# Performance work log

Hardware: AMD Instinct MI355X
Metric: run time of the kernel (lower is better)

## Reference

```python
import jax, jax.numpy as jnp
import numpy as np

B, S, N = 64, 32, 128            # batch, seq_len, padded nodes per graph
DV, DW, DH = 512, 300, 1024      # dim_v, dim_word, dim_hidden
CLS, T_CTRL, L = 1024, 12, 4     # cls_fc_dim, controller steps, stack_len
NQ, NA, NE, NATTR, M = 100, 28, 16, 1000, 6  # vocabs, edge cats, attrs, num modules
# module order: 0 NoOp, 1 Find(push), 2 Transform, 3 Filter, 4 And, 5 Describe

def _valid_mat():
    m = np.zeros((L, M), dtype=np.float32)
    for s in range(L):
        m[s, 0] = 1.0
        m[s, 1] = 1.0 if s < L - 1 else 0.0
        m[s, 2] = 1.0 if s >= 1 else 0.0
        m[s, 3] = 1.0 if s >= 1 else 0.0
        m[s, 4] = 1.0 if s >= 2 else 0.0
        m[s, 5] = 1.0 if s >= 1 else 0.0
    return jnp.asarray(m)

VALID_MAT = _valid_mat()

def setup_inputs() -> dict:
    key = jax.random.key(0)
    ks = jax.random.split(key, 24)
    nrm = lambda k, sh, sc: jax.random.normal(k, sh, jnp.float32) * sc
    inp = {}
    inp['questions'] = jax.random.randint(ks[0], (B, S), 0, NQ)
    inp['questions_len'] = jax.random.randint(ks[1], (B,), 8, S + 1)
    inp['conn'] = (jax.random.uniform(ks[2], (B, N, N)) < 0.2).astype(jnp.float32)
    inp['cat_mat'] = jax.random.randint(ks[3], (B, N, N), 0, NE)
    inp['v_idx'] = jax.random.randint(ks[4], (B, N), 0, NATTR)
    inp['attr_emb'] = nrm(ks[5], (NATTR, DV), 1.0 / np.sqrt(DV))
    inp['edge_cat_vectors'] = nrm(ks[6], (NE, DV), 1.0 / np.sqrt(DV))
    inp['enc_emb'] = nrm(ks[7], (NQ, DW), 1.0 / np.sqrt(DW))
    inp['Wx'] = nrm(ks[8], (DW, 4 * DH), 1.0 / np.sqrt(DW))
    inp['Wh'] = nrm(ks[9], (DH, 4 * DH), 1.0 / np.sqrt(DH))
    inp['b_lstm'] = jnp.zeros((4 * DH,), jnp.float32)
    inp['W_cq'] = nrm(ks[10], (2 * DH, DH), 1.0 / np.sqrt(2 * DH))
    inp['b_cq'] = jnp.zeros((DH,), jnp.float32)
    inp['W_mod'] = nrm(ks[11], (DH, M), 1.0 / np.sqrt(DH))
    inp['W_att'] = nrm(ks[12], (DH, DH), 1.0 / np.sqrt(DH))
    inp['W_q'] = nrm(ks[13], (DH, DV), np.sqrt(2.0 / DH))
    inp['b_q'] = jnp.zeros((DV,), jnp.float32)
    inp['W_find'] = nrm(ks[14], (DV, DV), 1.0 / np.sqrt(DV))
    inp['W_desc'] = nrm(ks[15], (DV, DV), 1.0 / np.sqrt(DV))
    inp['W_cls1'] = nrm(ks[16], (DV + DH, CLS), np.sqrt(2.0 / (DV + DH)))
    inp['b_cls1'] = jnp.zeros((CLS,), jnp.float32)
    inp['W_cls2'] = nrm(ks[17], (CLS, NA), np.sqrt(2.0 / CLS))
    inp['b_cls2'] = jnp.zeros((NA,), jnp.float32)
    return inp

def _read(st, p):
    return jnp.einsum('bnl,bl->bn', st, p)

def _write(st, p, a):
    pe = p[:, None, :]
    return a[:, :, None] * pe + st * (1.0 - pe)

def _ptr_fw(p):
    q = jnp.concatenate([jnp.zeros_like(p[:, :1]), p[:, :-1]], axis=1)
    return q.at[:, -1].add(p[:, -1])

def _ptr_bw(p):
    q = jnp.concatenate([p[:, 1:], jnp.zeros_like(p[:, :1])], axis=1)
    return q.at[:, 0].add(p[:, 0])

def reference(questions, questions_len, conn, cat_mat, v_idx, attr_emb,
              edge_cat_vectors, enc_emb, Wx, Wh, b_lstm, W_cq, b_cq, W_mod,
              W_att, W_q, b_q, W_find, W_desc, W_cls1, b_cls1, W_cls2, b_cls2):
    # ---- question encoder: embedding + LSTM over time-major sequence ----
    emb = enc_emb[questions].transpose(1, 0, 2)  # [S,B,DW]

    def lstm_step(carry, x):
        h, c = carry
        g = x @ Wx + h @ Wh + b_lstm
        i, f, gg, o = jnp.split(g, 4, axis=-1)
        c = jax.nn.sigmoid(f) * c + jax.nn.sigmoid(i) * jnp.tanh(gg)
        h = jax.nn.sigmoid(o) * jnp.tanh(c)
        return (h, c), h

    init = (jnp.zeros((B, DH), jnp.float32), jnp.zeros((B, DH), jnp.float32))
    _, outs = jax.lax.scan(lstm_step, init, emb)            # [S,B,DH]
    outs_b = outs.transpose(1, 0, 2)                         # [B,S,DH]
    q_hidden = outs_b[jnp.arange(B), questions_len - 1]      # last valid state

    mask = jnp.arange(S)[:, None] < questions_len[None, :]   # [S,B]
    feat = attr_emb[v_idx]                                   # [B,N,DV]
    bidx = jnp.arange(B)[:, None, None]

    att_stack = jnp.zeros((B, N, L), jnp.float32)
    stack_ptr = jnp.zeros((B, L), jnp.float32).at[:, 0].set(1.0)
    mem = jnp.zeros((B, DV), jnp.float32)
    c_ctrl = jnp.zeros((B, DH), jnp.float32)
    inv_sqrt_dv = 1.0 / np.sqrt(DV)

    for t in range(T_CTRL):
        # ---- controller step: module distribution + textual attention ----
        cq = jnp.tanh(jnp.concatenate([c_ctrl, q_hidden], axis=1) @ W_cq + b_cq)
        module_prob = jax.nn.softmax(cq @ W_mod, axis=-1)     # [B,M]
        al = jnp.einsum('sbh,bh->sb', outs, cq @ W_att)
        cv = jax.nn.softmax(jnp.where(mask, al, -1e9), axis=0)
        c_ctrl = jnp.einsum('sb,sbh->bh', cv, outs)
        c_i = jax.nn.relu(c_ctrl @ W_q + b_q)                 # [B,DV]

        # ---- validity masking of module distribution ----
        validity = jnp.round(stack_ptr @ VALID_MAT)           # [B,M]
        mp = module_prob * validity
        s = jnp.sum(mp, axis=1, keepdims=True)
        mp = mp / jnp.where(s > 0, s, 1.0)

        # ---- run every module, soft-average by module prob ----
        a_find = jax.nn.sigmoid(jnp.einsum('bnd,bd->bn', feat @ W_find, c_i) * inv_sqrt_dv)
        a_in = _read(att_stack, stack_ptr)
        # Transform: edge-category-weighted message passing on graph
        we = jax.nn.softmax(c_i @ edge_cat_vectors.T, axis=-1)   # [B,NE]
        ew = we[bidx, cat_mat] * conn                            # [B,N,N]
        a_trans = jnp.minimum(jnp.einsum('bij,bj->bi', ew, a_in), 1.0)
        p_fw = _ptr_fw(stack_ptr)
        p_bw = _ptr_bw(stack_ptr)
        a_prev = _read(att_stack, p_bw)
        pooled = jnp.einsum('bn,bnd->bd', a_in, feat) / (jnp.sum(a_in, 1, keepdims=True) + 1e-6)
        res = [
            (att_stack, stack_ptr, mem),                                  # NoOp
            (_write(att_stack, p_fw, a_find), p_fw, mem),                 # Find (push)
            (_write(att_stack, stack_ptr, a_trans), stack_ptr, mem),      # Transform
            (_write(att_stack, stack_ptr, a_in * a_find), stack_ptr, mem),# Filter
            (_write(att_stack, p_bw, jnp.minimum(a_prev, a_in)), p_bw, mem),  # And (pop)
            (att_stack, p_bw, pooled @ W_desc),                           # Describe
        ]
        att_stack = jnp.einsum('bm,mbnl->bnl', mp, jnp.stack([r[0] for r in res]))
        stack_ptr = jnp.einsum('bm,mbl->bl', mp, jnp.stack([r[1] for r in res]))
        mem = jnp.einsum('bm,mbd->bd', mp, jnp.stack([r[2] for r in res]))

    final = jnp.concatenate([mem, q_hidden], axis=1)
    h1 = jax.nn.relu(final @ W_cls1 + b_cls1)
    logits = h1 @ W_cls2 + b_cls2
    return logits
```

## Files before the change

### kernel.cpp

```cpp
#include <hip/hip_runtime.h>
#include <math.h>

#define B 64
#define S 32
#define NN 128
#define DV 512
#define DW 300
#define DH 1024
#define CLS 1024
#define T_CTRL 12
#define LL 4
#define NA 28
#define NE 16
#define MM 6

__device__ __forceinline__ float sigmoidf_(float x) { return 1.0f / (1.0f + expf(-x)); }

template<bool TRANS, class AF, class WF>
__device__ __forceinline__ void gemm_core(int kbeg, int Kc, AF loadA, WF loadW,
                                          float* part, int Cld, int orow) {
  __shared__ float Ast[2][64 * 36];
  __shared__ float Ws[2][32 * 64];
  const int tid = threadIdx.x;
  const int j0 = blockIdx.x * 64;
  const int ntiles = Kc >> 5;
  const int rg = tid & 15, cg = tid >> 4;
  float4 av[2], wv[2];

  auto fetch = [&](int kt) {
    #pragma unroll
    for (int i2 = 0; i2 < 2; ++i2) {
      int idx = tid + i2 * 256;
      av[i2] = loadA(idx >> 3, kt + (idx & 7) * 4);
    }
    #pragma unroll
    for (int i2 = 0; i2 < 2; ++i2) {
      int idx = tid + i2 * 256;
      if (!TRANS) wv[i2] = loadW(kt + (idx >> 4), j0 + (idx & 15) * 4);
      else        wv[i2] = loadW(j0 + (idx >> 3), kt + (idx & 7) * 4);
    }
  };
  auto commit = [&](int buf) {
    #pragma unroll
    for (int i2 = 0; i2 < 2; ++i2) {
      int idx = tid + i2 * 256;
      *(float4*)&Ast[buf][(idx >> 3) * 36 + (idx & 7) * 4] = av[i2];
    }
    #pragma unroll
    for (int i2 = 0; i2 < 2; ++i2) {
      int idx = tid + i2 * 256;
      if (!TRANS) {
        *(float4*)&Ws[buf][(idx >> 4) * 64 + (idx & 15) * 4] = wv[i2];
      } else {
        int jloc = idx >> 3, k4 = (idx & 7) * 4;
        Ws[buf][(k4 + 0) * 64 + jloc] = wv[i2].x;
        Ws[buf][(k4 + 1) * 64 + jloc] = wv[i2].y;
        Ws[buf][(k4 + 2) * 64 + jloc] = wv[i2].z;
        Ws[buf][(k4 + 3) * 64 + jloc] = wv[i2].w;
      }
    }
  };

  float acc[4][4] = {};
  fetch(kbeg);
  commit(0);
  __syncthreads();
  for (int i = 0; i < ntiles; ++i) {
    if (i + 1 < ntiles) fetch(kbeg + (i + 1) * 32);
    const float* As = &Ast[i & 1][0];
    const float* Wp = &Ws[i & 1][0];
    #pragma unroll
    for (int kq = 0; kq < 8; ++kq) {
      float4 a0 = *(const float4*)&As[(rg     ) * 36 + kq * 4];
      float4 a1 = *(const float4*)&As[(rg + 16) * 36 + kq * 4];
      float4 a2 = *(const float4*)&As[(rg + 32) * 36 + kq * 4];
      float4 a3 = *(const float4*)&As[(rg + 48) * 36 + kq * 4];
      float4 w0 = *(const float4*)&Wp[(kq * 4 + 0) * 64 + cg * 4];
      float4 w1 = *(const float4*)&Wp[(kq * 4 + 1) * 64 + cg * 4];
      float4 w2 = *(const float4*)&Wp[(kq * 4 + 2) * 64 + cg * 4];
      float4 w3 = *(const float4*)&Wp[(kq * 4 + 3) * 64 + cg * 4];
      #define STEP(m, AV) \
        acc[m][0]=fmaf(AV.x,w0.x,acc[m][0]); acc[m][1]=fmaf(AV.x,w0.y,acc[m][1]); \
        acc[m][2]=fmaf(AV.x,w0.z,acc[m][2]); acc[m][3]=fmaf(AV.x,w0.w,acc[m][3]); \
        acc[m][0]=fmaf(AV.y,w1.x,acc[m][0]); acc[m][1]=fmaf(AV.y,w1.y,acc[m][1]); \
        acc[m][2]=fmaf(AV.y,w1.z,acc[m][2]); acc[m][3]=fmaf(AV.y,w1.w,acc[m][3]); \
        acc[m][0]=fmaf(AV.z,w2.x,acc[m][0]); acc[m][1]=fmaf(AV.z,w2.y,acc[m][1]); \
        acc[m][2]=fmaf(AV.z,w2.z,acc[m][2]); acc[m][3]=fmaf(AV.z,w2.w,acc[m][3]); \
        acc[m][0]=fmaf(AV.w,w3.x,acc[m][0]); acc[m][1]=fmaf(AV.w,w3.y,acc[m][1]); \
        acc[m][2]=fmaf(AV.w,w3.z,acc[m][2]); acc[m][3]=fmaf(AV.w,w3.w,acc[m][3]);
      STEP(0, a0) STEP(1, a1) STEP(2, a2) STEP(3, a3)
      #undef STEP
    }
    if (i + 1 < ntiles) { __syncthreads(); commit((i + 1) & 1); __syncthreads(); }
  }
  float* op = part + (size_t)orow * 64 * Cld + j0 + cg * 4;
  #pragma unroll
  for (int m = 0; m < 4; ++m)
    *(float4*)&op[(size_t)(rg + 16 * m) * Cld] = make_float4(acc[m][0], acc[m][1], acc[m][2], acc[m][3]);
}

__global__ void init_kernel(float* c_lstm, float* c_ctrl, float* att_stack, float* mem, float* sptr) {
  int idx = blockIdx.x * 256 + threadIdx.x;
  if (idx < B * DH) { c_lstm[idx] = 0.f; c_ctrl[idx] = 0.f; }
  if (idx < B * NN * LL) att_stack[idx] = 0.f;
  if (idx < B * DV) mem[idx] = 0.f;
  if (idx < B * LL) sptr[idx] = ((idx & (LL - 1)) == 0) ? 1.f : 0.f;
}

__global__ void embq_kernel(const int* __restrict__ questions, const float* __restrict__ enc_emb,
                            float* __restrict__ embq) {
  int row = blockIdx.x;
  int t = row >> 6, b = row & 63;
  int qid = questions[b * S + t];
  int c = threadIdx.x;
  embq[(size_t)row * 320 + c] = (c < DW) ? enc_emb[(size_t)qid * DW + c] : 0.f;
}

__global__ __launch_bounds__(256) void xpre_kernel(const float* __restrict__ embq,
                                                   const float* __restrict__ Wx,
                                                   float* __restrict__ Xbuf) {
  int t = blockIdx.y, ch = blockIdx.z;
  auto Al = [&](int r, int k) -> float4 {
    return *(const float4*)&embq[(size_t)(t * 64 + r) * 320 + k];
  };
  auto Wl = [&](int k, int j) -> float4 {
    if (k < 300) return *(const float4*)&Wx[(size_t)k * 4096 + j];
    return make_float4(0.f, 0.f, 0.f, 0.f);
  };
  gemm_core<false>(ch * 160, 160, Al, Wl, Xbuf + (size_t)t * 524288 + (size_t)ch * 262144, 4096, 0);
}

__global__ __launch_bounds__(256) void f2_kernel(const float* __restrict__ attr_emb,
                                                 const float* __restrict__ W_find,
                                                 float* __restrict__ F2) {
  auto Al = [&](int r, int k) -> float4 {
    int gr = blockIdx.y * 64 + r;
    if (gr > 999) gr = 999;
    return *(const float4*)&attr_emb[(size_t)gr * 512 + k];
  };
  auto Wl = [&](int k, int j) -> float4 { return *(const float4*)&W_find[(size_t)k * 512 + j]; };
  gemm_core<false>(0, 512, Al, Wl, F2, 512, blockIdx.y);
}

__global__ __launch_bounds__(256) void lstm_gemm_kernel(const float* __restrict__ h_prev,
                                                        const float* __restrict__ Wh,
                                                        float* __restrict__ part,
                                                        const float* __restrict__ embq,
                                                        const float* __restrict__ Wx,
                                                        float* __restrict__ Xbuf, int t) {
  if (blockIdx.y < 8) {
    auto Al = [&](int r, int k) -> float4 { return *(const float4*)&h_prev[(size_t)r * 1024 + k]; };
    auto Wl = [&](int k, int j) -> float4 { return *(const float4*)&Wh[(size_t)k * 4096 + j]; };
    gemm_core<false>(blockIdx.y * 128, 128, Al, Wl, part, 4096, blockIdx.y);
  } else {
    if (t == 31) return;
    int ch = blockIdx.y - 8;
    auto Al = [&](int r, int k) -> float4 {
      return *(const float4*)&embq[(size_t)((t + 1) * 64 + r) * 320 + k];
    };
    auto Wl = [&](int k, int j) -> float4 {
      if (k < 300) return *(const float4*)&Wx[(size_t)k * 4096 + j];
      return make_float4(0.f, 0.f, 0.f, 0.f);
    };
    gemm_core<false>(ch * 160, 160, Al, Wl,
                     Xbuf + (size_t)((t + 1) & 1) * 524288 + (size_t)ch * 262144, 4096, 0);
  }
}

__global__ __launch_bounds__(256) void lstm_gate_kernel(const float* __restrict__ part, int SK,
                                                        const float* __restrict__ px,
                                                        const float* __restrict__ b_lstm,
                                                        float* __restrict__ h_out, float* __restrict__ c_st) {
  int idx = blockIdx.x * 256 + threadIdx.x;
  int b = idx >> 10, j = idx & 1023;
  const float* x0 = px + (size_t)b * 4096;
  const float* x1 = px + 262144 + (size_t)b * 4096;
  float gi = x0[j] + x1[j];
  float gf = x0[1024 + j] + x1[1024 + j];
  float gg = x0[2048 + j] + x1[2048 + j];
  float go = x0[3072 + j] + x1[3072 + j];
  const float* pb = part + (size_t)b * 4096;
  for (int c = 0; c < SK; ++c) {
    const float* p = pb + (size_t)c * 262144;
    gi += p[j]; gf += p[1024 + j]; gg += p[2048 + j]; go += p[3072 + j];
  }
  gi += b_lstm[j]; gf += b_lstm[1024 + j]; gg += b_lstm[2048 + j]; go += b_lstm[3072 + j];
  float c = sigmoidf_(gf) * c_st[idx] + sigmoidf_(gi) * tanhf(gg);
  h_out[idx] = sigmoidf_(go) * tanhf(c);
  c_st[idx] = c;
}

__global__ __launch_bounds__(256) void c1_kernel(const float* __restrict__ c_ctrl,
                                                 const float* __restrict__ outs, const int* __restrict__ qlen,
                                                 const float* __restrict__ W_cq, float* __restrict__ partA,
                                                 const float* __restrict__ partE, const float* __restrict__ mp,
                                                 float* __restrict__ mem, int do_epi) {
  if (blockIdx.x == 16) {
    if (!do_epi) return;
    int t0 = blockIdx.y * 256 + threadIdx.x;
    #pragma unroll
    for (int i = 0; i < 4; ++i) {
      int f4 = t0 + i * 2048;
      int b = f4 >> 7, j = (f4 & 127) * 4;
      const float* m = &mp[b * 6];
      float s04 = m[0] + m[1] + m[2] + m[3] + m[4];
      float4 s = make_float4(0.f, 0.f, 0.f, 0.f);
      for (int c = 0; c < 8; ++c) {
        float4 v = *(const float4*)&partE[(size_t)c * 32768 + b * 512 + j];
        s.x += v.x; s.y += v.y; s.z += v.z; s.w += v.w;
      }
      float4 o = *(const float4*)&mem[b * 512 + j];
      o.x = s04 * o.x + m[5] * s.x; o.y = s04 * o.y + m[5] * s.y;
      o.z = s04 * o.z + m[5] * s.z; o.w = s04 * o.w + m[5] * s.w;
      *(float4*)&mem[b * 512 + j] = o;
    }
    return;
  }
  auto Al = [&](int r, int k) -> float4 {
    if (k < 1024) return *(const float4*)&c_ctrl[r * 1024 + k];
    int tq = qlen[r] - 1;
    return *(const float4*)&outs[(size_t)tq * 65536 + r * 1024 + (k - 1024)];
  };
  auto Wl = [&](int k, int j) -> float4 { return *(const float4*)&W_cq[(size_t)k * 1024 + j]; };
  gemm_core<false>(blockIdx.y * 256, 256, Al, Wl, partA, 1024, blockIdx.y);
}

__global__ __launch_bounds__(256) void c2_kernel(const float* __restrict__ partA,
                                                 const float* __restrict__ b_cq,
                                                 const float* __restrict__ W_att,
                                                 const float* __restrict__ W_mod,
                                                 float* __restrict__ partB) {
  auto Al = [&](int r, int k) -> float4 {
    float4 s = *(const float4*)&b_cq[k];
    for (int c = 0; c < 8; ++c) {
      float4 v = *(const float4*)&partA[(size_t)c * 65536 + r * 1024 + k];
      s.x += v.x; s.y += v.y; s.z += v.z; s.w += v.w;
    }
    return make_float4(tanhf(s.x), tanhf(s.y), tanhf(s.z), tanhf(s.w));
  };
  auto Wl = [&](int k, int j) -> float4 {
    if (j < 1024) return *(const float4*)&W_att[(size_t)k * 1024 + j];
    float v[4];
    #pragma unroll
    for (int i = 0; i < 4; ++i) {
      int jj = j + i;
      v[i] = (jj < 1030) ? W_mod[(size_t)k * 6 + (jj - 1024)] : 0.f;
    }
    return make_float4(v[0], v[1], v[2], v[3]);
  };
  gemm_core<false>(blockIdx.y * 64, 64, Al, Wl, partB, 1088, blockIdx.y);
}

__global__ __launch_bounds__(256) void attn_kernel(const float* __restrict__ partB,
                                                   const float* __restrict__ outs,
                                                   const int* __restrict__ qlen,
                                                   float* __restrict__ c_ctrl) {
  int b = blockIdx.x >> 2, hq = blockIdx.x & 3;
  int tid = threadIdx.x;
  __shared__ float aw[DH];
  __shared__ float alv[S];
  __shared__ float cvs[S];
  {
    int c4 = tid * 4;
    float4 s = make_float4(0.f, 0.f, 0.f, 0.f);
    for (int c = 0; c < 16; ++c) {
      float4 v = *(const float4*)&partB[(size_t)c * 69632 + b * 1088 + c4];
      s.x += v.x; s.y += v.y; s.z += v.z; s.w += v.w;
    }
    *(float4*)&aw[c4] = s;
  }
  __syncthreads();
  {
    int wv = tid >> 6, lane = tid & 63;
    #pragma unroll
    for (int u = 0; u < 4; ++u) {
      int s2 = wv * 4 + u;
      const float4* orow = (const float4*)&outs[(size_t)s2 * 65536 + b * 1024];
      float pr = 0.f;
      #pragma unroll
      for (int q = 0; q < 4; ++q) {
        float4 f = orow[lane + 64 * q];
        float4 w = *(const float4*)&aw[(lane + 64 * q) * 4];
        pr += f.x * w.x + f.y * w.y + f.z * w.z + f.w * w.w;
      }
      #pragma unroll
      for (int off = 32; off > 0; off >>= 1) pr += __shfl_xor(pr, off);
      if (lane == 0) alv[s2] = pr;
    }
  }
  __syncthreads();
  if (tid < 64) {
    int len = qlen[b];
    float v = (tid < S && tid < len) ? alv[tid] : -1e9f;
    float mx = v;
    #pragma unroll
    for (int off = 32; off > 0; off >>= 1) mx = fmaxf(mx, __shfl_xor(mx, off));
    float e = (tid < S && tid < len) ? expf(v - mx) : 0.f;
    float sm = e;
    #pragma unroll
    for (int off = 32; off > 0; off >>= 1) sm += __shfl_xor(sm, off);
    if (tid < S) cvs[tid] = e / sm;
  }
  __syncthreads();
  {
    int h = hq * 256 + tid;
    float a = 0.f;
    #pragma unroll 8
    for (int s2 = 0; s2 < S; ++s2)
      a = fmaf(cvs[s2], outs[(size_t)s2 * 65536 + b * 1024 + h], a);
    c_ctrl[b * 1024 + h] = a;
  }
}

__global__ __launch_bounds__(256) void c4_kernel(const float* __restrict__ c_ctrl,
                                                 const float* __restrict__ W_q,
                                                 float* __restrict__ partC) {
  auto Al = [&](int r, int k) -> float4 { return *(const float4*)&c_ctrl[r * 1024 + k]; };
  auto Wl = [&](int k, int j) -> float4 { return *(const float4*)&W_q[(size_t)k * 512 + j]; };
  gemm_core<false>(blockIdx.y * 64, 64, Al, Wl, partC, 512, blockIdx.y);
}

__global__ __launch_bounds__(256) void prep_kernel(const float* __restrict__ partC,
                                                   const float* __restrict__ partB,
                                                   const float* __restrict__ b_q,
                                                   const float* __restrict__ edge_cat,
                                                   const float* __restrict__ sptr_in,
                                                   const float* __restrict__ att_stack,
                                                   float* __restrict__ c_i, float* __restrict__ we,
                                                   float* __restrict__ mp, float* __restrict__ spv,
                                                   float* __restrict__ ain, float* __restrict__ aw4,
                                                   float* __restrict__ asum) {
  int b = blockIdx.x, tid = threadIdx.x;
  __shared__ float ci[512];
  __shared__ float lds[64];
  for (int col = tid; col < 512; col += 256) {
    float s = b_q[col];
    for (int c = 0; c < 16; ++c) s += partC[(size_t)c * 32768 + b * 512 + col];
    s = fmaxf(s, 0.f);
    ci[col] = s;
    c_i[b * 512 + col] = s;
  }
  if (tid < MM) {
    float s = 0.f;
    for (int c = 0; c < 16; ++c) s += partB[(size_t)c * 69632 + b * 1088 + 1024 + tid];
    lds[16 + tid] = s;
  }
  __syncthreads();
  {
    int wv = tid >> 6, lane = tid & 63;
    for (int e = wv; e < NE; e += 4) {
      const float* er = &edge_cat[(size_t)e * 512];
      float p = 0.f;
      #pragma unroll
      for (int q = 0; q < 8; ++q) p = fmaf(ci[lane + 64 * q], er[lane + 64 * q], p);
      #pragma unroll
      for (int off = 32; off > 0; off >>= 1) p += __shfl_xor(p, off);
      if (lane == 0) lds[e] = p;
    }
  }
  __syncthreads();
  if (tid == 0) {
    float mx = lds[0];
    for (int e = 1; e < NE; ++e) mx = fmaxf(mx, lds[e]);
    float sm = 0.f, ex[NE];
    for (int e = 0; e < NE; ++e) { ex[e] = expf(lds[e] - mx); sm += ex[e]; }
    for (int e = 0; e < NE; ++e) we[b * NE + e] = ex[e] / sm;
    float mx2 = lds[16];
    for (int m = 1; m < MM; ++m) mx2 = fmaxf(mx2, lds[16 + m]);
    float e6[MM], sm2 = 0.f;
    for (int m = 0; m < MM; ++m) { e6[m] = expf(lds[16 + m] - mx2); sm2 += e6[m]; }
    float p0 = sptr_in[b * 4 + 0], p1 = sptr_in[b * 4 + 1];
    float p2 = sptr_in[b * 4 + 2], p3 = sptr_in[b * 4 + 3];
    float sp[12];
    sp[0] = p0; sp[1] = p1; sp[2] = p2; sp[3] = p3;
    sp[4] = 0.f;      sp[5] = p0; sp[6] = p1; sp[7] = p2 + p3;
    sp[8] = p0 + p1;  sp[9] = p2; sp[10] = p3; sp[11] = 0.f;
    for (int i = 0; i < 12; ++i) { spv[b * 12 + i] = sp[i]; lds[22 + i] = sp[i]; }
    float val[MM];
    val[0] = rintf(p0 + p1 + p2 + p3);
    val[1] = rintf(p0 + p1 + p2);
    val[2] = rintf(p1 + p2 + p3);
    val[3] = val[2];
    val[4] = rintf(p2 + p3);
    val[5] = val[2];
    float mpv[MM], ssum = 0.f;
    #pragma unroll
    for (int m = 0; m < MM; ++m) { mpv[m] = (e6[m] / sm2) * val[m]; ssum += mpv[m]; }
    float inv = (ssum > 0.f) ? 1.f / ssum : 1.f;
    #pragma unroll
    for (int m = 0; m < MM; ++m) mp[b * MM + m] = mpv[m] * inv;
  }
  __syncthreads();
  if (tid < 128) {
    float4 st = *(const float4*)&att_stack[(b * NN + tid) * LL];
    float ainv = st.x * lds[22] + st.y * lds[23] + st.z * lds[24] + st.w * lds[25];
    float ap   = st.x * lds[30] + st.y * lds[31] + st.z * lds[32] + st.w * lds[33];
    ain[b * NN + tid] = ainv;
    aw4[b * NN + tid] = fminf(ap, ainv);
    float t2 = ainv;
    #pragma unroll
    for (int off = 32; off > 0; off >>= 1) t2 += __shfl_xor(t2, off);
    if ((tid & 63) == 0) lds[40 + (tid >> 6)] = t2;
  }
  __syncthreads();
  if (tid == 0) asum[b] = lds[40] + lds[41] + 1e-6f;
}

__global__ __launch_bounds__(256) void stackf_kernel(const int* __restrict__ v_idx,
                                                     const float* __restrict__ attr_emb,
                                                     const float* __restrict__ F2,
                                                     const float* __restrict__ c_i,
                                                     const float* __restrict__ we,
                                                     const int* __restrict__ cat_mat,
                                                     const float* __restrict__ conn,
                                                     const float* __restrict__ ain,
                                                     const float* __restrict__ asum,
                                                     float* __restrict__ afind,
                                                     float* __restrict__ atr,
                                                     float* __restrict__ pooled) {
  int job = blockIdx.x, tid = threadIdx.x;
  __shared__ float lds[192];
  if (job < 2048) {
    int gw = job * 4 + (tid >> 6);
    int b = gw >> 7, n = gw & 127, lane = tid & 63;
    int vid = v_idx[b * NN + n];
    const float4* fp = (const float4*)&F2[(size_t)vid * DV];
    const float4* up = (const float4*)&c_i[(size_t)b * DV];
    float pr = 0.f;
    #pragma unroll
    for (int q = 0; q < 2; ++q) {
      float4 f = fp[lane + 64 * q], u = up[lane + 64 * q];
      pr += f.x * u.x + f.y * u.y + f.z * u.z + f.w * u.w;
    }
    #pragma unroll
    for (int off = 32; off > 0; off >>= 1) pr += __shfl_xor(pr, off);
    if (lane == 0) afind[b * NN + n] = sigmoidf_(pr * 0.04419417382415922f);
  } else if (job < 2560) {
    int j2 = job - 2048;
    int b = j2 >> 3, ig = j2 & 7;
    if (tid < 128) lds[tid] = ain[b * NN + tid];
    else if (tid < 144) lds[tid] = we[b * NE + tid - 128];
    __syncthreads();
    int i = ig * 16 + (tid >> 4);
    const int* crow = &cat_mat[((size_t)b * NN + i) * NN];
    const float* nrow = &conn[((size_t)b * NN + i) * NN];
    float a = 0.f;
    #pragma unroll
    for (int q = 0; q < 8; ++q) {
      int j = (tid & 15) + 16 * q;
      a = fmaf(lds[128 + crow[j]] * nrow[j], lds[j], a);
    }
    a += __shfl_xor(a, 1); a += __shfl_xor(a, 2); a += __shfl_xor(a, 4); a += __shfl_xor(a, 8);
    if ((tid & 15) == 0) atr[b * NN + i] = fminf(a, 1.f);
  } else {
    int j3 = job - 2560;
    int b = j3 >> 1, d = (j3 & 1) * 256 + tid;
    int* vidL = (int*)&lds[128];
    if (tid < 128) { lds[tid] = ain[b * NN + tid]; vidL[tid] = v_idx[b * NN + tid]; }
    __syncthreads();
    float a = 0.f;
    #pragma unroll 4
    for (int n = 0; n < NN; ++n)
      a = fmaf(lds[n], attr_emb[(size_t)vidL[n] * DV + d], a);
    pooled[b * DV + d] = a / asum[b];
  }
}

__global__ __launch_bounds__(256) void c7u_kernel(const float* __restrict__ pooled,
                                                  const float* __restrict__ W_desc,
                                                  float* __restrict__ partE,
                                                  const float* __restrict__ spv,
                                                  const float* __restrict__ mp,
                                                  const float* __restrict__ afind,
                                                  const float* __restrict__ ain,
                                                  const float* __restrict__ atr,
                                                  const float* __restrict__ aw4,
                                                  float* __restrict__ att_stack,
                                                  float* __restrict__ sptr) {
  int tid = threadIdx.x;
  if (blockIdx.y < 8) {
    auto Al = [&](int r, int k) -> float4 { return *(const float4*)&pooled[r * 512 + k]; };
    auto Wl = [&](int k, int j) -> float4 { return *(const float4*)&W_desc[(size_t)k * 512 + j]; };
    gemm_core<false>(blockIdx.y * 64, 64, Al, Wl, partE, 512, blockIdx.y);
    return;
  }
  int b = (blockIdx.y - 8) * 8 + blockIdx.x;
  __shared__ float sp[12], smp[MM];
  if (tid < 12) sp[tid] = spv[b * 12 + tid];
  else if (tid < 12 + MM) smp[tid - 12] = mp[b * MM + (tid - 12)];
  __syncthreads();
  #pragma unroll
  for (int i = 0; i < 2; ++i) {
    int e = tid + i * 256;
    int n = e >> 2, l = e & 3;
    float st = att_stack[(b * NN + n) * LL + l];
    float keep = smp[0] + smp[5] + smp[1] * (1.f - sp[4 + l]) + (smp[2] + smp[3]) * (1.f - sp[l])
               + smp[4] * (1.f - sp[8 + l]);
    float add = sp[4 + l] * smp[1] * afind[b * NN + n]
              + sp[l] * (smp[2] * atr[b * NN + n] + smp[3] * ain[b * NN + n] * afind[b * NN + n])
              + sp[8 + l] * smp[4] * aw4[b * NN + n];
    att_stack[(b * NN + n) * LL + l] = keep * st + add;
  }
  if (tid < LL)
    sptr[b * LL + tid] = (smp[0] + smp[2] + smp[3]) * sp[tid] + smp[1] * sp[4 + tid]
                       + (smp[4] + smp[5]) * sp[8 + tid];
}

__global__ __launch_bounds__(256) void cl1_kernel(const float* __restrict__ partE,
                                                  const float* __restrict__ mp,
                                                  const float* __restrict__ mem,
                                                  const float* __restrict__ outs,
                                                  const int* __restrict__ qlen,
                                                  const float* __restrict__ W_cls1,
                                                  float* __restrict__ partH) {
  auto Al = [&](int r, int k) -> float4 {
    if (k < 512) {
      float4 s = make_float4(0.f, 0.f, 0.f, 0.f);
      for (int c = 0; c < 8; ++c) {
        float4 v = *(const float4*)&partE[(size_t)c * 32768 + r * 512 + k];
        s.x += v.x; s.y += v.y; s.z += v.z; s.w += v.w;
      }
      const float* m = &mp[r * 6];
      float s04 = m[0] + m[1] + m[2] + m[3] + m[4];
      float4 o = *(const float4*)&mem[r * 512 + k];
      return make_float4(s04 * o.x + m[5] * s.x, s04 * o.y + m[5] * s.y,
                         s04 * o.z + m[5] * s.z, s04 * o.w + m[5] * s.w);
    }
    int tq = qlen[r] - 1;
    return *(const float4*)&outs[(size_t)tq * 65536 + r * 1024 + (k - 512)];
  };
  auto Wl = [&](int k, int j) -> float4 { return *(const float4*)&W_cls1[(size_t)k * 1024 + j]; };
  gemm_core<false>(blockIdx.y * 192, 192, Al, Wl, partH, 1024, blockIdx.y);
}

__global__ __launch_bounds__(256) void cl2_kernel(const float* __restrict__ partH,
                                                  const float* __restrict__ b_cls1,
                                                  const float* __restrict__ W_cls2,
                                                  float* __restrict__ partJ) {
  auto Al = [&](int r, int k) -> float4 {
    float4 s = *(const float4*)&b_cls1[k];
    for (int c = 0; c < 8; ++c) {
      float4 v = *(const float4*)&partH[(size_t)c * 65536 + r * 1024 + k];
      s.x += v.x; s.y += v.y; s.z += v.z; s.w += v.w;
    }
    return make_float4(fmaxf(s.x, 0.f), fmaxf(s.y, 0.f), fmaxf(s.z, 0.f), fmaxf(s.w, 0.f));
  };
  auto Wl = [&](int k, int j) -> float4 {
    float v[4];
    #pragma unroll
    for (int i = 0; i < 4; ++i) { int jj = j + i; v[i] = (jj < NA) ? W_cls2[(size_t)k * NA + jj] : 0.f; }
    return make_float4(v[0], v[1], v[2], v[3]);
  };
  gemm_core<false>(blockIdx.y * 128, 128, Al, Wl, partJ, 64, blockIdx.y);
}

__global__ void cl3_kernel(const float* __restrict__ partJ, const float* __restrict__ b_cls2,
                           float* __restrict__ logits) {
  int idx = blockIdx.x * 256 + threadIdx.x;
  if (idx >= B * NA) return;
  int r = idx / NA, j = idx - r * NA;
  float s = b_cls2[j];
  for (int c = 0; c < 8; ++c) s += partJ[(size_t)c * 4096 + r * 64 + j];
  logits[idx] = s;
}

extern "C" void kernel_launch(void* const* d_in, const int* in_sizes, int n_in,
                              void* d_out, int out_size, void* d_ws, size_t ws_size,
                              hipStream_t stream) {
  const int*   questions = (const int*)d_in[0];
  const int*   qlen      = (const int*)d_in[1];
  const float* conn      = (const float*)d_in[2];
  const int*   cat_mat   = (const int*)d_in[3];
  const int*   v_idx     = (const int*)d_in[4];
  const float* attr_emb  = (const float*)d_in[5];
  const float* edge_cat  = (const float*)d_in[6];
  const float* enc_emb   = (const float*)d_in[7];
  const float* Wx        = (const float*)d_in[8];
  const float* Wh        = (const float*)d_in[9];
  const float* b_lstm    = (const float*)d_in[10];
  const float* W_cq      = (const float*)d_in[11];
  const float* b_cq      = (const float*)d_in[12];
  const float* W_mod     = (const float*)d_in[13];
  const float* W_att     = (const float*)d_in[14];
  const float* W_q       = (const float*)d_in[15];
  const float* b_q       = (const float*)d_in[16];
  const float* W_find    = (const float*)d_in[17];
  const float* W_desc    = (const float*)d_in[18];
  const float* W_cls1    = (const float*)d_in[19];
  const float* b_cls1    = (const float*)d_in[20];
  const float* W_cls2    = (const float*)d_in[21];
  const float* b_cls2    = (const float*)d_in[22];
  float* logits = (float*)d_out;

  float* w = (float*)d_ws;
  size_t off = 0;
  float* outs      = w + off; off += (size_t)S * B * DH;
  float* embq      = w + off; off += (size_t)S * B * 320;
  float* Xbuf      = w + off; off += 2 * 2 * 262144;
  float* F2        = w + off; off += 1024 * 512;
  float* share     = w + off; off += 2457600;
  float* partE     = w + off; off += 262144;
  float* partH     = w + off; off += 524288;
  float* partJ     = w + off; off += 32768;
  float* c_ctrl    = w + off; off += B * DH;
  float* c_lstm    = w + off; off += B * DH;
  float* ci_buf    = w + off; off += B * DV;
  float* we_buf    = w + off; off += B * NE;
  float* mp_buf    = w + off; off += B * MM;
  float* spv_buf   = w + off; off += B * 12;
  float* ain_buf   = w + off; off += B * NN;
  float* aw4_buf   = w + off; off += B * NN;
  float* afind_buf = w + off; off += B * NN;
  float* atr_buf   = w + off; off += B * NN;
  float* asum_buf  = w + off; off += B;
  float* att_stack = w + off; off += B * NN * LL;
  float* sptr_buf  = w + off; off += B * LL;
  float* mem       = w + off; off += B * DV;
  float* pooled    = w + off; off += B * DV;

  float* partLSTM = share;
  float* partA = share;
  float* partB = share + 524288;
  float* partC = share + 1638400;

  init_kernel<<<256, 256, 0, stream>>>(c_lstm, c_ctrl, att_stack, mem, sptr_buf);
  embq_kernel<<<S * B, 320, 0, stream>>>(questions, enc_emb, embq);
  xpre_kernel<<<dim3(64, 2, 2), 256, 0, stream>>>(embq, Wx, Xbuf);
  f2_kernel<<<dim3(8, 16), 256, 0, stream>>>(attr_emb, W_find, F2);

  lstm_gate_kernel<<<(B * DH) / 256, 256, 0, stream>>>(partLSTM, 0, Xbuf, b_lstm, outs, c_lstm);
  for (int t = 1; t < S; ++t) {
    lstm_gemm_kernel<<<dim3(64, 10), 256, 0, stream>>>(outs + (size_t)(t - 1) * B * DH, Wh,
                                                       partLSTM, embq, Wx, Xbuf, t);
    lstm_gate_kernel<<<(B * DH) / 256, 256, 0, stream>>>(partLSTM, 8, Xbuf + (size_t)(t & 1) * 524288,
                                                         b_lstm, outs + (size_t)t * B * DH, c_lstm);
  }

  for (int it = 0; it < T_CTRL; ++it) {
    c1_kernel<<<dim3(17, 8), 256, 0, stream>>>(c_ctrl, outs, qlen, W_cq, partA,
                                               partE, mp_buf, mem, it > 0 ? 1 : 0);
    c2_kernel<<<dim3(17, 16), 256, 0, stream>>>(partA, b_cq, W_att, W_mod, partB);
    attn_kernel<<<256, 256, 0, stream>>>(partB, outs, qlen, c_ctrl);
    c4_kernel<<<dim3(8, 16), 256, 0, stream>>>(c_ctrl, W_q, partC);
    prep_kernel<<<64, 256, 0, stream>>>(partC, partB, b_q, edge_cat, sptr_buf, att_stack,
                                        ci_buf, we_buf, mp_buf, spv_buf, ain_buf, aw4_buf, asum_buf);
    stackf_kernel<<<2688, 256, 0, stream>>>(v_idx, attr_emb, F2, ci_buf, we_buf, cat_mat, conn,
                                            ain_buf, asum_buf, afind_buf, atr_buf, pooled);
    c7u_kernel<<<dim3(8, 16), 256, 0, stream>>>(pooled, W_desc, partE, spv_buf, mp_buf,
                                                afind_buf, ain_buf, atr_buf, aw4_buf,
                                                att_stack, sptr_buf);
  }

  cl1_kernel<<<dim3(16, 8), 256, 0, stream>>>(partE, mp_buf, mem, outs, qlen, W_cls1, partH);
  cl2_kernel<<<dim3(1, 8), 256, 0, stream>>>(partH, b_cls1, W_cls2, partJ);
  cl3_kernel<<<7, 256, 0, stream>>>(partJ, b_cls2, logits);
}
```

Before: 1.575 ms.

## Precompute all LSTM input projections upfront and fuse W_q GEMM into prep kernel

Replaces the per-step overlapped input-projection GEMM with a single up-front GEMM over all 32 timesteps, stored in a full-size X buffer, so each recurrent step launches only the Wh GEMM. It also removes the separate c4 split-K GEMM kernel and computes c_ctrl·W_q directly inside prep_kernel with a per-batch-row dot-product loop. This cuts one launch per controller iteration and the partial-sum traffic. The cost is a scalar 1024x512 matvec per block in prep, run on only 64 blocks, which may be slower than the tiled GEMM it replaces.

```diff
diff --git a/kernel.cpp b/kernel.cpp
--- a/kernel.cpp
+++ b/kernel.cpp
@@ -116,18 +116,17 @@
   embq[(size_t)row * 320 + c] = (c < DW) ? enc_emb[(size_t)qid * DW + c] : 0.f;
 }
 
-__global__ __launch_bounds__(256) void xpre_kernel(const float* __restrict__ embq,
-                                                   const float* __restrict__ Wx,
-                                                   float* __restrict__ Xbuf) {
-  int t = blockIdx.y, ch = blockIdx.z;
+__global__ __launch_bounds__(256) void xgemm_kernel(const float* __restrict__ embq,
+                                                    const float* __restrict__ Wx,
+                                                    float* __restrict__ X) {
   auto Al = [&](int r, int k) -> float4 {
-    return *(const float4*)&embq[(size_t)(t * 64 + r) * 320 + k];
+    return *(const float4*)&embq[(size_t)(blockIdx.y * 64 + r) * 320 + k];
   };
   auto Wl = [&](int k, int j) -> float4 {
     if (k < 300) return *(const float4*)&Wx[(size_t)k * 4096 + j];
     return make_float4(0.f, 0.f, 0.f, 0.f);
   };
-  gemm_core<false>(ch * 160, 160, Al, Wl, Xbuf + (size_t)t * 524288 + (size_t)ch * 262144, 4096, 0);
+  gemm_core<false>(0, 320, Al, Wl, X, 4096, blockIdx.y);
 }
 
 __global__ __launch_bounds__(256) void f2_kernel(const float* __restrict__ attr_emb,
@@ -144,41 +143,20 @@
 
 __global__ __launch_bounds__(256) void lstm_gemm_kernel(const float* __restrict__ h_prev,
                                                         const float* __restrict__ Wh,
-                                                        float* __restrict__ part,
-                                                        const float* __restrict__ embq,
-                                                        const float* __restrict__ Wx,
-                                                        float* __restrict__ Xbuf, int t) {
-  if (blockIdx.y < 8) {
-    auto Al = [&](int r, int k) -> float4 { return *(const float4*)&h_prev[(size_t)r * 1024 + k]; };
-    auto Wl = [&](int k, int j) -> float4 { return *(const float4*)&Wh[(size_t)k * 4096 + j]; };
-    gemm_core<false>(blockIdx.y * 128, 128, Al, Wl, part, 4096, blockIdx.y);
-  } else {
-    if (t == 31) return;
-    int ch = blockIdx.y - 8;
-    auto Al = [&](int r, int k) -> float4 {
-      return *(const float4*)&embq[(size_t)((t + 1) * 64 + r) * 320 + k];
-    };
-    auto Wl = [&](int k, int j) -> float4 {
-      if (k < 300) return *(const float4*)&Wx[(size_t)k * 4096 + j];
-      return make_float4(0.f, 0.f, 0.f, 0.f);
-    };
-    gemm_core<false>(ch * 160, 160, Al, Wl,
-                     Xbuf + (size_t)((t + 1) & 1) * 524288 + (size_t)ch * 262144, 4096, 0);
-  }
+                                                        float* __restrict__ part) {
+  auto Al = [&](int r, int k) -> float4 { return *(const float4*)&h_prev[(size_t)r * 1024 + k]; };
+  auto Wl = [&](int k, int j) -> float4 { return *(const float4*)&Wh[(size_t)k * 4096 + j]; };
+  gemm_core<false>(blockIdx.y * 128, 128, Al, Wl, part, 4096, blockIdx.y);
 }
 
 __global__ __launch_bounds__(256) void lstm_gate_kernel(const float* __restrict__ part, int SK,
-                                                        const float* __restrict__ px,
+                                                        const float* __restrict__ X, int t,
                                                         const float* __restrict__ b_lstm,
                                                         float* __restrict__ h_out, float* __restrict__ c_st) {
   int idx = blockIdx.x * 256 + threadIdx.x;
   int b = idx >> 10, j = idx & 1023;
-  const float* x0 = px + (size_t)b * 4096;
-  const float* x1 = px + 262144 + (size_t)b * 4096;
-  float gi = x0[j] + x1[j];
-  float gf = x0[1024 + j] + x1[1024 + j];
-  float gg = x0[2048 + j] + x1[2048 + j];
-  float go = x0[3072 + j] + x1[3072 + j];
+  const float* xr = X + ((size_t)t * 64 + b) * 4096;
+  float gi = xr[j], gf = xr[1024 + j], gg = xr[2048 + j], go = xr[3072 + j];
   const float* pb = part + (size_t)b * 4096;
   for (int c = 0; c < SK; ++c) {
     const float* p = pb + (size_t)c * 262144;
@@ -312,17 +290,10 @@
   }
 }
 
-__global__ __launch_bounds__(256) void c4_kernel(const float* __restrict__ c_ctrl,
-                                                 const float* __restrict__ W_q,
-                                                 float* __restrict__ partC) {
-  auto Al = [&](int r, int k) -> float4 { return *(const float4*)&c_ctrl[r * 1024 + k]; };
-  auto Wl = [&](int k, int j) -> float4 { return *(const float4*)&W_q[(size_t)k * 512 + j]; };
-  gemm_core<false>(blockIdx.y * 64, 64, Al, Wl, partC, 512, blockIdx.y);
-}
-
-__global__ __launch_bounds__(256) void prep_kernel(const float* __restrict__ partC,
+__global__ __launch_bounds__(256) void prep_kernel(const float* __restrict__ c_ctrl,
+                                                   const float* __restrict__ W_q,
+                                                   const float* __restrict__ b_q,
                                                    const float* __restrict__ partB,
-                                                   const float* __restrict__ b_q,
                                                    const float* __restrict__ edge_cat,
                                                    const float* __restrict__ sptr_in,
                                                    const float* __restrict__ att_stack,
@@ -331,19 +302,28 @@
                                                    float* __restrict__ ain, float* __restrict__ aw4,
                                                    float* __restrict__ asum) {
   int b = blockIdx.x, tid = threadIdx.x;
+  __shared__ float cc[1024];
   __shared__ float ci[512];
   __shared__ float lds[64];
-  for (int col = tid; col < 512; col += 256) {
-    float s = b_q[col];
-    for (int c = 0; c < 16; ++c) s += partC[(size_t)c * 32768 + b * 512 + col];
-    s = fmaxf(s, 0.f);
-    ci[col] = s;
-    c_i[b * 512 + col] = s;
+  {
+    float4 v = *(const float4*)&c_ctrl[b * 1024 + tid * 4];
+    *(float4*)&cc[tid * 4] = v;
   }
   if (tid < MM) {
     float s = 0.f;
     for (int c = 0; c < 16; ++c) s += partB[(size_t)c * 69632 + b * 1088 + 1024 + tid];
     lds[16 + tid] = s;
+  }
+  __syncthreads();
+  #pragma unroll
+  for (int half = 0; half < 2; ++half) {
+    int j = half * 256 + tid;
+    float s = b_q[j];
+    #pragma unroll 8
+    for (int k = 0; k < 1024; ++k) s = fmaf(cc[k], W_q[(size_t)k * 512 + j], s);
+    s = fmaxf(s, 0.f);
+    ci[j] = s;
+    c_i[b * 512 + j] = s;
   }
   __syncthreads();
   {
@@ -596,7 +576,7 @@
   size_t off = 0;
   float* outs      = w + off; off += (size_t)S * B * DH;
   float* embq      = w + off; off += (size_t)S * B * 320;
-  float* Xbuf      = w + off; off += 2 * 2 * 262144;
+  float* X         = w + off; off += (size_t)S * B * 4096;
   float* F2        = w + off; off += 1024 * 512;
   float* share     = w + off; off += 2457600;
   float* partE     = w + off; off += 262144;
@@ -621,19 +601,17 @@
   float* partLSTM = share;
   float* partA = share;
   float* partB = share + 524288;
-  float* partC = share + 1638400;
 
   init_kernel<<<256, 256, 0, stream>>>(c_lstm, c_ctrl, att_stack, mem, sptr_buf);
   embq_kernel<<<S * B, 320, 0, stream>>>(questions, enc_emb, embq);
-  xpre_kernel<<<dim3(64, 2, 2), 256, 0, stream>>>(embq, Wx, Xbuf);
+  xgemm_kernel<<<dim3(64, 32), 256, 0, stream>>>(embq, Wx, X);
   f2_kernel<<<dim3(8, 16), 256, 0, stream>>>(attr_emb, W_find, F2);
 
-  lstm_gate_kernel<<<(B * DH) / 256, 256, 0, stream>>>(partLSTM, 0, Xbuf, b_lstm, outs, c_lstm);
+  lstm_gate_kernel<<<(B * DH) / 256, 256, 0, stream>>>(partLSTM, 0, X, 0, b_lstm, outs, c_lstm);
   for (int t = 1; t < S; ++t) {
-    lstm_gemm_kernel<<<dim3(64, 10), 256, 0, stream>>>(outs + (size_t)(t - 1) * B * DH, Wh,
-                                                       partLSTM, embq, Wx, Xbuf, t);
-    lstm_gate_kernel<<<(B * DH) / 256, 256, 0, stream>>>(partLSTM, 8, Xbuf + (size_t)(t & 1) * 524288,
-                                                         b_lstm, outs + (size_t)t * B * DH, c_lstm);
+    lstm_gemm_kernel<<<dim3(64, 8), 256, 0, stream>>>(outs + (size_t)(t - 1) * B * DH, Wh, partLSTM);
+    lstm_gate_kernel<<<(B * DH) / 256, 256, 0, stream>>>(partLSTM, 8, X, t, b_lstm,
+                                                         outs + (size_t)t * B * DH, c_lstm);
   }
 
   for (int it = 0; it < T_CTRL; ++it) {
@@ -641,8 +619,7 @@
                                                partE, mp_buf, mem, it > 0 ? 1 : 0);
     c2_kernel<<<dim3(17, 16), 256, 0, stream>>>(partA, b_cq, W_att, W_mod, partB);
     attn_kernel<<<256, 256, 0, stream>>>(partB, outs, qlen, c_ctrl);
-    c4_kernel<<<dim3(8, 16), 256, 0, stream>>>(c_ctrl, W_q, partC);
-    prep_kernel<<<64, 256, 0, stream>>>(partC, partB, b_q, edge_cat, sptr_buf, att_stack,
+    prep_kernel<<<64, 256, 0, stream>>>(c_ctrl, W_q, b_q, partB, edge_cat, sptr_buf, att_stack,
                                         ci_buf, we_buf, mp_buf, spv_buf, ain_buf, aw4_buf, asum_buf);
     stackf_kernel<<<2688, 256, 0, stream>>>(v_idx, attr_emb, F2, ci_buf, we_buf, cat_mat, conn,
                                             ain_buf, asum_buf, afind_buf, atr_buf, pooled);
```

After: 2.527 ms. +60.5%, slower.
